# Kernel tuning notes

Hardware: AMD Instinct MI355X
Metric: run time of the kernel (lower is better)

## Reference

```python
import jax, jax.numpy as jnp
import numpy as np

D_MODEL = 1024
NHEAD = 8
HEAD_DIM = D_MODEL // NHEAD
D_FF = 4096
EPS_ATTN = 1e-6
EPS_LN = 1e-5


def _layernorm(x, g, b):
    mu = jnp.mean(x, axis=-1, keepdims=True)
    var = jnp.var(x, axis=-1, keepdims=True)
    return (x - mu) * jax.lax.rsqrt(var + EPS_LN) * g + b


def _linear_attention(q, k, v):
    # q,k,v: [N, L, H, D]
    Q = jax.nn.elu(q) + 1.0
    K = jax.nn.elu(k) + 1.0
    v_length = v.shape[1]
    v = v / v_length
    KV = jnp.einsum('nshd,nshv->nhdv', K, v)           # [N,H,D,D]
    Z = 1.0 / (jnp.einsum('nlhd,nhd->nlh', Q, K.sum(axis=1)) + EPS_ATTN)
    out = jnp.einsum('nlhd,nhdv,nlh->nlhv', Q, KV, Z) * v_length
    return out


def setup_inputs() -> dict:
    key = jax.random.key(0)
    ks = jax.random.split(key, 12)
    s = 1.0 / np.sqrt(D_MODEL)
    sf = 1.0 / np.sqrt(D_FF)
    return {
        'x': jax.random.normal(ks[0], (2, 4096, D_MODEL), jnp.float32),
        'wq': jax.random.normal(ks[1], (D_MODEL, D_MODEL), jnp.float32) * s,
        'wk': jax.random.normal(ks[2], (D_MODEL, D_MODEL), jnp.float32) * s,
        'wv': jax.random.normal(ks[3], (D_MODEL, D_MODEL), jnp.float32) * s,
        'w1': jax.random.normal(ks[4], (D_FF, D_MODEL), jnp.float32) * s,
        'b1': jnp.zeros((D_FF,), jnp.float32),
        'w2': jax.random.normal(ks[5], (D_MODEL, D_FF), jnp.float32) * sf,
        'b2': jnp.zeros((D_MODEL,), jnp.float32),
        'g1': jnp.ones((D_MODEL,), jnp.float32),
        'be1': jnp.zeros((D_MODEL,), jnp.float32),
        'g2': jnp.ones((D_MODEL,), jnp.float32),
        'be2': jnp.zeros((D_MODEL,), jnp.float32),
    }


def reference(x, wq, wk, wv, w1, b1, w2, b2, g1, be1, g2, be2):
    N, L, C = x.shape
    # pre-norm self attention
    x2 = _layernorm(x, g1, be1)
    q = (x2 @ wq.T).reshape(N, L, NHEAD, HEAD_DIM)
    k = (x2 @ wk.T).reshape(N, L, NHEAD, HEAD_DIM)
    v = (x2 @ wv.T).reshape(N, L, NHEAD, HEAD_DIM)
    msg = _linear_attention(q, k, v).reshape(N, L, C)
    x = x + msg
    # MLP block
    x2 = _layernorm(x, g2, be2)
    h = jax.nn.gelu(x2 @ w1.T + b1, approximate=False)
    x = x + (h @ w2.T + b2)
    return x
```

## Files before the change

kernel.cpp:

```cpp
#include <hip/hip_runtime.h>
#include <hip/hip_bf16.h>
#include <math.h>

typedef __bf16 bf16x8 __attribute__((ext_vector_type(8)));
typedef float f32x4 __attribute__((ext_vector_type(4)));

#define DEVI __device__ __forceinline__

DEVI void gload_lds16(const __bf16* g, __bf16* l) {
    __builtin_amdgcn_global_load_lds(
        (const __attribute__((address_space(1))) void*)g,
        (__attribute__((address_space(3))) void*)l, 16, 0, 0);
}

__global__ void sniff_kernel(const unsigned short* __restrict__ x, int* flags) {
    const int tid = threadIdx.x;
    const unsigned short u = x[tid * 2];
    const int e = (u >> 7) & 0xFF;
    const int zero = (u == 0) ? 1 : 0;
    const int sane = ((e >= 0x71 && e <= 0x8E) || ((u & 0x7FFF) == 0)) ? 1 : 0;
    const unsigned long long mz = __ballot(zero != 0);
    const unsigned long long ms = __ballot(sane != 0);
    __shared__ int wz[4], wsn[4];
    if ((tid & 63) == 0) { wz[tid >> 6] = __popcll(mz); wsn[tid >> 6] = __popcll(ms); }
    __syncthreads();
    if (tid == 0) {
        const int nz = wz[0] + wz[1] + wz[2] + wz[3];
        const int ns = wsn[0] + wsn[1] + wsn[2] + wsn[3];
        flags[0] = (nz >= 192 || ns < 128) ? 1 : 0;
    }
}

__global__ __launch_bounds__(256) void convert_kernel(const void* __restrict__ src,
                                                      __bf16* __restrict__ dst, int n,
                                                      const int* __restrict__ flags) {
    const int i = (blockIdx.x * 256 + threadIdx.x) * 8;
    if (i >= n) return;
    if (flags[0]) {
        const float* s = (const float*)src;
        bf16x8 o;
#pragma unroll
        for (int j = 0; j < 8; j++) o[j] = (__bf16)s[i + j];
        *(bf16x8*)(dst + i) = o;
    } else {
        *(uint4*)(dst + i) = *(const uint4*)((const __bf16*)src + i);
    }
}

template <typename T>
__global__ __launch_bounds__(256) void ln_kernel(const T* __restrict__ x,
                                                 const __bf16* __restrict__ g,
                                                 const __bf16* __restrict__ b,
                                                 __bf16* __restrict__ out) {
    const size_t row = blockIdx.x;
    const T* xr = x + row * 1024;
    const int tid = threadIdx.x;
    float v[4];
#pragma unroll
    for (int i = 0; i < 4; i++) v[i] = (float)xr[tid * 4 + i];
    float s = v[0] + v[1] + v[2] + v[3];
    float s2 = v[0] * v[0] + v[1] * v[1] + v[2] * v[2] + v[3] * v[3];
#pragma unroll
    for (int m = 32; m >= 1; m >>= 1) {
        s += __shfl_xor(s, m, 64);
        s2 += __shfl_xor(s2, m, 64);
    }
    __shared__ float rs[4], rs2[4];
    const int wave = tid >> 6, lane = tid & 63;
    if (lane == 0) { rs[wave] = s; rs2[wave] = s2; }
    __syncthreads();
    s = rs[0] + rs[1] + rs[2] + rs[3];
    s2 = rs2[0] + rs2[1] + rs2[2] + rs2[3];
    const float mu = s * (1.0f / 1024.0f);
    const float var = s2 * (1.0f / 1024.0f) - mu * mu;
    const float inv = rsqrtf(var + 1e-5f);
#pragma unroll
    for (int i = 0; i < 4; i++) {
        const int c = tid * 4 + i;
        out[row * 1024 + c] = (__bf16)((v[i] - mu) * inv * (float)g[c] + (float)b[c]);
    }
}

enum { EP_NONE = 0, EP_ELU1 = 1, EP_BIAS_GELU = 2, EP_BIAS_RES = 3, EP_QKV = 4 };

#define STG256(DST, P0, P1, KOFF)                         \
    do {                                                  \
        gload_lds16((P0) + (KOFF), &DST[tid * 8]);        \
        gload_lds16((P1) + (KOFF), &DST[4096 + tid * 8]); \
    } while (0)

#define MFMA4x4(AV, BV, FRB)                                                   \
    do {                                                                       \
        _Pragma("unroll") for (int f_ = 0; f_ < 4; f_++)                       \
            _Pragma("unroll") for (int c_ = 0; c_ < 4; c_++)                   \
                acc[(FRB) + f_][c_] = __builtin_amdgcn_mfma_f32_16x16x32_bf16( \
                    AV[f_], BV[c_], acc[(FRB) + f_][c_], 0, 0, 0);             \
    } while (0)

#define ITER256(RA0, RA1, RB0, RB1, SA0m, SA1m, SB0m, SB1m, TN, DO_STAGE, VM1) \
    do {                                                                       \
        bf16x8 a_[4];                                                          \
                                    \
        asm volatile("s_waitcnt vmcnt(4)" ::: "memory");                       \
        __builtin_amdgcn_s_barrier();                                          \
        __builtin_amdgcn_sched_barrier(0);                                     \
        _Pragma("unroll") for (int f_ = 0; f_ < 4; f_++)                       \
            b0[f_] = *(const bf16x8*)&RB0[boff[f_]];                           \
        _Pragma("unroll") for (int f_ = 0; f_ < 4; f_++)                       \
            a_[f_] = *(const bf16x8*)&RA0[aoff[f_]];                           \
        if (DO_STAGE) STG256(SA0m, sA0, sA1, (TN) * 64);                       \
        asm volatile("s_waitcnt lgkmcnt(0)" ::: "memory");                     \
        __builtin_amdgcn_sched_barrier(0);                                     \
        __builtin_amdgcn_s_setprio(1);                                         \
        MFMA4x4(a_, b0, 0);                                                    \
        __builtin_amdgcn_s_setprio(0);                                         \
                                    \
        asm volatile("s_waitcnt vmcnt(" #VM1 ")" ::: "memory");                \
        __builtin_amdgcn_s_barrier();                                          \
        __builtin_amdgcn_sched_barrier(0);                                     \
        _Pragma("unroll") for (int f_ = 0; f_ < 4; f_++)                       \
            b1[f_] = *(const bf16x8*)&RB1[boff[f_]];                           \
        _Pragma("unroll") for (int f_ = 0; f_ < 4; f_++)                       \
            a_[f_] = *(const bf16x8*)&RA1[aoff[f_]];                           \
        if (DO_STAGE) STG256(SB0m, sB0, sB1, (TN) * 64);                       \
        asm volatile("s_waitcnt lgkmcnt(0)" ::: "memory");                     \
        __builtin_amdgcn_sched_barrier(0);                                     \
        __builtin_amdgcn_s_setprio(1);                                         \
        MFMA4x4(a_, b1, 0);                                                    \
        __builtin_amdgcn_s_setprio(0);                                         \
                              \
        __builtin_amdgcn_s_barrier();                                          \
        __builtin_amdgcn_sched_barrier(0);                                     \
        _Pragma("unroll") for (int f_ = 0; f_ < 4; f_++)                       \
            a_[f_] = *(const bf16x8*)&RA0[aoff[4 + f_]];                       \
        if (DO_STAGE) STG256(SA1m, sA0, sA1, (TN) * 64 + 32);                  \
        asm volatile("s_waitcnt lgkmcnt(0)" ::: "memory");                     \
        __builtin_amdgcn_sched_barrier(0);                                     \
        __builtin_amdgcn_s_setprio(1);                                         \
        MFMA4x4(a_, b0, 4);                                                    \
        __builtin_amdgcn_s_setprio(0);                                         \
                              \
        __builtin_amdgcn_s_barrier();                                          \
        __builtin_amdgcn_sched_barrier(0);                                     \
        _Pragma("unroll") for (int f_ = 0; f_ < 4; f_++)                       \
            a_[f_] = *(const bf16x8*)&RA1[aoff[4 + f_]];                       \
        if (DO_STAGE) STG256(SB1m, sB0, sB1, (TN) * 64 + 32);                  \
        asm volatile("s_waitcnt lgkmcnt(0)" ::: "memory");                     \
        __builtin_amdgcn_sched_barrier(0);                                     \
        __builtin_amdgcn_s_setprio(1);                                         \
        MFMA4x4(a_, b1, 4);                                                    \
        __builtin_amdgcn_s_setprio(0);                                         \
    } while (0)

template <int EP>
__global__ __launch_bounds__(512, 2) void gemm256(
    const __bf16* __restrict__ A, const __bf16* __restrict__ B,
    const __bf16* __restrict__ bias, __bf16* __restrict__ out2,
    __bf16* __restrict__ out3, __bf16* __restrict__ C, int M, int N, int K) {
    const int gx = gridDim.x, gy = gridDim.y;
    int bm = blockIdx.y, bn = blockIdx.x;
    {
        const int nwg = gx * gy;
        const int bid = bm * gx + bn;
        if ((gx & 7) == 0 && (nwg & 63) == 0) {
            const int perx = nwg >> 3;
            const int gid = (bid & 7) * perx + (bid >> 3);
            const int stg = gid >> 6, pos = gid & 63;
            const int stw = gx >> 3;
            bm = (stg / stw) * 8 + (pos >> 3);
            bn = (stg % stw) * 8 + (pos & 7);
        } else if ((nwg & 7) == 0) {
            const int perx = nwg >> 3;
            const int gid = (bid & 7) * perx + (bid >> 3);
            bm = gid / gx;
            bn = gid % gx;
        }
    }
    const int tid = threadIdx.x;
    const int wave = tid >> 6, lane = tid & 63;
    const int wr = wave >> 2, wc = wave & 3;
    const int lm = lane & 15, lq = lane >> 4;

    __shared__ __align__(16) __bf16 A0k0[8192];
    __shared__ __align__(16) __bf16 A0k1[8192];
    __shared__ __align__(16) __bf16 B0k0[8192];
    __shared__ __align__(16) __bf16 B0k1[8192];
    __shared__ __align__(16) __bf16 A1k0[8192];
    __shared__ __align__(16) __bf16 A1k1[8192];
    __shared__ __align__(16) __bf16 B1k0[8192];
    __shared__ __align__(16) __bf16 B1k1[8192];

    f32x4 acc[8][4] = {};
    bf16x8 b0[4], b1[4];

    int aoff[8], boff[4];
#pragma unroll
    for (int fr = 0; fr < 8; fr++) {
        const int row = wr * 128 + fr * 16 + lm;
        aoff[fr] = row * 32 + ((lq ^ (lm & 3)) << 3);
    }
#pragma unroll
    for (int fc = 0; fc < 4; fc++) {
        const int row = wc * 64 + fc * 16 + lm;
        boff[fc] = row * 32 + ((lq ^ (lm & 3)) << 3);
    }

    const int srow = tid >> 2;
    const int sg = (((tid & 3) ^ ((tid >> 2) & 3)) << 3);
    const __bf16* sA0 = A + (size_t)(bm * 256 + srow) * K + sg;
    const __bf16* sA1 = sA0 + (size_t)128 * K;
    const __bf16* sB0 = B + (size_t)(bn * 256 + srow) * K + sg;
    const __bf16* sB1 = sB0 + (size_t)128 * K;

    const int nt = K >> 6;

    STG256(A0k0, sA0, sA1, 0);
    STG256(B0k0, sB0, sB1, 0);
    STG256(A0k1, sA0, sA1, 32);
    STG256(B0k1, sB0, sB1, 32);

    int t = 0;
    for (; t + 2 < nt; t += 2) {
        ITER256(A0k0, A0k1, B0k0, B0k1, A1k0, A1k1, B1k0, B1k1, t + 1, true, 2);
        ITER256(A1k0, A1k1, B1k0, B1k1, A0k0, A0k1, B0k0, B0k1, t + 2, true, 2);
    }
    ITER256(A0k0, A0k1, B0k0, B0k1, A1k0, A1k1, B1k0, B1k1, t + 1, true, 2);
    ITER256(A1k0, A1k1, B1k0, B1k1, A0k0, A0k1, B0k0, B0k1, 0, false, 0);

    const int rowb = bm * 256 + wr * 128 + lq * 4;
    const int colb = bn * 256 + wc * 64 + lm;
#pragma unroll
    for (int fr = 0; fr < 8; fr++) {
#pragma unroll
        for (int fc = 0; fc < 4; fc++) {
            const int col = colb + fc * 16;
#pragma unroll
            for (int r = 0; r < 4; r++) {
                const int row = rowb + fr * 16 + r;
                float v = acc[fr][fc][r];
                if (EP == EP_QKV) {
                    float vv = (col < 2048) ? ((v > 0.0f) ? (v + 1.0f) : expf(v)) : v;
                    __bf16* dst = (col < 1024) ? C : (col < 2048) ? out2 : out3;
                    dst[(size_t)row * 1024 + (col & 1023)] = (__bf16)vv;
                } else {
                    v += (float)bias[col];
                    v = 0.5f * v * (1.0f + erff(v * 0.70710678118654752f));
                    C[(size_t)row * N + col] = (__bf16)v;
                }
            }
        }
    }
}

#define READMM(RA, RB)                                                           \
    do {                                                                         \
        bf16x8 af_[4], bfv_[4];                                                  \
        _Pragma("unroll") for (int i_ = 0; i_ < 4; i_++) {                       \
            af_[i_] = *(const bf16x8*)&RA[(wm * 64 + i_ * 16 + lm) * 32 + swz];  \
            bfv_[i_] = *(const bf16x8*)&RB[(wn * 64 + i_ * 16 + lm) * 32 + swz]; \
        }                                                                        \
        _Pragma("unroll") for (int i_ = 0; i_ < 4; i_++)                         \
            _Pragma("unroll") for (int j_ = 0; j_ < 4; j_++)                     \
                acc[i_][j_] = __builtin_amdgcn_mfma_f32_16x16x32_bf16(           \
                    af_[i_], bfv_[j_], acc[i_][j_], 0, 0, 0);                    \
    } while (0)

#define KBODY(RA, RB, SA, SB, TS, WAITN)                           \
    do {                                                           \
        asm volatile("s_waitcnt vmcnt(" #WAITN ")" ::: "memory");  \
        __builtin_amdgcn_s_barrier();                              \
        __builtin_amdgcn_sched_barrier(0);                         \
        if ((TS) < nt) {                                           \
            const int k0_ = (TS) << 5;                             \
            gload_lds16(pa0 + k0_, &SA[tid * 8]);                  \
            gload_lds16(pa1 + k0_, &SA[2048 + tid * 8]);           \
            gload_lds16(pb0 + k0_, &SB[tid * 8]);                  \
            gload_lds16(pb1 + k0_, &SB[2048 + tid * 8]);           \
        }                                                          \
        __builtin_amdgcn_s_setprio(1);                             \
        READMM(RA, RB);                                            \
        __builtin_amdgcn_s_setprio(0);                             \
    } while (0)

template <int EP, typename OutT>
__global__ __launch_bounds__(256, 3) void gemm_bt(
    const __bf16* __restrict__ A, const __bf16* __restrict__ B,
    const __bf16* __restrict__ bias, const float* __restrict__ resid,
    OutT* __restrict__ C, int M, int N, int K) {
    const int gx = gridDim.x, gy = gridDim.y;
    int bm = blockIdx.y, bn = blockIdx.x;
    {
        const int nwg = gx * gy;
        if ((gx & 7) == 0 && (nwg & 63) == 0) {
            const int bid = bm * gx + bn;
            const int perx = nwg >> 3;
            const int gid = (bid & 7) * perx + (bid >> 3);
            const int stg = gid >> 6, pos = gid & 63;
            const int stw = gx >> 3;
            bm = (stg / stw) * 8 + (pos >> 3);
            bn = (stg % stw) * 8 + (pos & 7);
        }
    }
    const int tid = threadIdx.x;
    const int wave = tid >> 6, lane = tid & 63;
    const int wm = wave & 1, wn = wave >> 1;
    const int lm = lane & 15, lq = lane >> 4;
    const int swz = (lq ^ ((lm >> 1) & 3)) * 8;

    __shared__ __align__(16) __bf16 As0[128 * 32];
    __shared__ __align__(16) __bf16 As1[128 * 32];
    __shared__ __align__(16) __bf16 As2[128 * 32];
    __shared__ __align__(16) __bf16 Bs0[128 * 32];
    __shared__ __align__(16) __bf16 Bs1[128 * 32];
    __shared__ __align__(16) __bf16 Bs2[128 * 32];

    f32x4 acc[4][4] = {};

    const int sr = tid >> 2;
    const int sc = (((tid & 3) ^ ((tid >> 3) & 3)) << 3);

    const __bf16* pa0 = A + (size_t)(bm * 128 + sr) * K + sc;
    const __bf16* pa1 = pa0 + (size_t)64 * K;
    const __bf16* pb0 = B + (size_t)(bn * 128 + sr) * K + sc;
    const __bf16* pb1 = pb0 + (size_t)64 * K;

    const int nt = K >> 5;

    gload_lds16(pa0, &As0[tid * 8]);
    gload_lds16(pa1, &As0[2048 + tid * 8]);
    gload_lds16(pb0, &Bs0[tid * 8]);
    gload_lds16(pb1, &Bs0[2048 + tid * 8]);
    if (nt > 1) {
        gload_lds16(pa0 + 32, &As1[tid * 8]);
        gload_lds16(pa1 + 32, &As1[2048 + tid * 8]);
        gload_lds16(pb0 + 32, &Bs1[tid * 8]);
        gload_lds16(pb1 + 32, &Bs1[2048 + tid * 8]);
    }

    int t = 0;
    for (; t + 2 < nt; t += 3) {
        KBODY(As0, Bs0, As2, Bs2, t + 2, 4);
        KBODY(As1, Bs1, As0, Bs0, t + 3, 4);
        KBODY(As2, Bs2, As1, Bs1, t + 4, 4);
    }
    if (t < nt) {
        asm volatile("s_waitcnt vmcnt(0)" ::: "memory");
        __builtin_amdgcn_s_barrier();
        __builtin_amdgcn_sched_barrier(0);
        READMM(As0, Bs0);
        t++;
        if (t < nt) { READMM(As1, Bs1); }
    }

    const int row0 = bm * 128 + wm * 64;
    const int col0 = bn * 128 + wn * 64;
#pragma unroll
    for (int i = 0; i < 4; i++) {
#pragma unroll
        for (int j = 0; j < 4; j++) {
            const int col = col0 + j * 16 + lm;
#pragma unroll
            for (int r = 0; r < 4; r++) {
                const int row = row0 + i * 16 + lq * 4 + r;
                float v = acc[i][j][r];
                if (EP == EP_ELU1) {
                    v = (v > 0.0f) ? (v + 1.0f) : expf(v);
                } else if (EP == EP_BIAS_GELU) {
                    v += (float)bias[col];
                    v = 0.5f * v * (1.0f + erff(v * 0.70710678118654752f));
                } else if (EP == EP_BIAS_RES) {
                    v += (float)bias[col];
                    v += resid[(size_t)row * N + col];
                }
                C[(size_t)row * N + col] = (OutT)v;
            }
        }
    }
}

__global__ __launch_bounds__(256) void kv_kernel(const __bf16* __restrict__ Kf,
                                                 const __bf16* __restrict__ Vf,
                                                 float* __restrict__ pkv,
                                                 float* __restrict__ pks) {
    const int nh = blockIdx.x, sc = blockIdx.y;
    const int n = nh >> 3, h = nh & 7;
    const int tid = threadIdx.x;
    const int tv = tid & 15, td = tid >> 4;
    __shared__ __align__(16) __bf16 Kt[32 * 128];
    __shared__ __align__(16) __bf16 Vt[32 * 128];
    float acc[8][8] = {};
    float ks[8] = {};
    const size_t rowbase = (size_t)n * 4096 + (size_t)sc * 256;
    for (int s0 = 0; s0 < 256; s0 += 32) {
#pragma unroll
        for (int rep = 0; rep < 2; rep++) {
            const int s = tid + rep * 256;
            const int r = s >> 4, cs = (s & 15) * 8;
            const size_t gidx = (rowbase + s0 + r) * 1024 + h * 128 + cs;
            *(bf16x8*)&Kt[r * 128 + cs] = *(const bf16x8*)&Kf[gidx];
            *(bf16x8*)&Vt[r * 128 + cs] = *(const bf16x8*)&Vf[gidx];
        }
        __syncthreads();
#pragma unroll 4
        for (int s = 0; s < 32; s++) {
            const bf16x8 k8 = *(const bf16x8*)&Kt[s * 128 + td * 8];
            const bf16x8 v8 = *(const bf16x8*)&Vt[s * 128 + tv * 8];
            float kk[8], vv[8];
#pragma unroll
            for (int i = 0; i < 8; i++) { kk[i] = (float)k8[i]; vv[i] = (float)v8[i]; }
#pragma unroll
            for (int i = 0; i < 8; i++) {
                ks[i] += kk[i];
#pragma unroll
                for (int j = 0; j < 8; j++) acc[i][j] += kk[i] * vv[j];
            }
        }
        __syncthreads();
    }
    float* dst = pkv + ((size_t)sc * 16 + nh) * 16384;
#pragma unroll
    for (int i = 0; i < 8; i++)
#pragma unroll
        for (int j = 0; j < 8; j++)
            dst[(td * 8 + i) * 128 + tv * 8 + j] = acc[i][j];
    if (tv == 0) {
        float* ds2 = pks + ((size_t)sc * 16 + nh) * 128;
#pragma unroll
        for (int i = 0; i < 8; i++) ds2[td * 8 + i] = ks[i];
    }
}

__global__ __launch_bounds__(256) void kv_reduce(const float* __restrict__ pkv,
                                                 const float* __restrict__ pks,
                                                 __bf16* __restrict__ kvb,
                                                 float* __restrict__ ksf) {
    const int idx = blockIdx.x * 256 + threadIdx.x;
    float s = 0.0f;
#pragma unroll
    for (int c = 0; c < 16; c++) s += pkv[(size_t)c * 262144 + idx];
    kvb[idx] = (__bf16)s;
    if (idx < 2048) {
        float t = 0.0f;
#pragma unroll
        for (int c = 0; c < 16; c++) t += pks[c * 2048 + idx];
        ksf[idx] = t;
    }
}

__global__ __launch_bounds__(256) void z_kernel(const __bf16* __restrict__ Qf,
                                                const float* __restrict__ ksf,
                                                float* __restrict__ zbuf) {
    const int idx = blockIdx.x * 256 + threadIdx.x;
    const int h = idx & 7;
    const size_t row = (size_t)(idx >> 3);
    const __bf16* q = Qf + row * 1024 + h * 128;
    const float* ks = ksf + ((size_t)((row >> 12) * 8 + h)) * 128;
    float s = 0.0f;
    for (int d = 0; d < 128; d += 8) {
        const bf16x8 q8 = *(const bf16x8*)&q[d];
#pragma unroll
        for (int j = 0; j < 8; j++) s += (float)q8[j] * ks[d + j];
    }
    zbuf[idx] = 1.0f / (s + 1e-6f);
}

__global__ __launch_bounds__(256, 2) void attn_out_kernel(
    const __bf16* __restrict__ x, const __bf16* __restrict__ Qf,
    const __bf16* __restrict__ kvb, const float* __restrict__ zbuf,
    float* __restrict__ xmid) {
    const int nh = blockIdx.x, lc = blockIdx.y;
    const int n = nh >> 3, h = nh & 7;
    const int tid = threadIdx.x;
    __shared__ __align__(16) __bf16 KVs[128 * 128];
    __shared__ __align__(16) __bf16 Qs[64 * 128];
    __shared__ float Zs[64];
    const __bf16* kv = kvb + (size_t)nh * 16384;
    for (int i = tid * 8; i < 16384; i += 2048)
        *(bf16x8*)&KVs[i] = *(const bf16x8*)&kv[i];
    const size_t gr0 = (size_t)n * 4096 + (size_t)lc * 64;
#pragma unroll
    for (int rep = 0; rep < 4; rep++) {
        const int s = tid + rep * 256;
        const int r = s >> 4, cs = (s & 15) * 8;
        *(bf16x8*)&Qs[r * 128 + cs] = *(const bf16x8*)&Qf[(gr0 + r) * 1024 + h * 128 + cs];
    }
    if (tid < 64) Zs[tid] = zbuf[(gr0 + tid) * 8 + h];
    __syncthreads();
    const int tv = (tid & 15) * 8;
    const int tr0 = (tid >> 4) * 4;
    float acc[4][8] = {};
    for (int d = 0; d < 128; d++) {
        const bf16x8 kv8 = *(const bf16x8*)&KVs[d * 128 + tv];
        float kf[8];
#pragma unroll
        for (int j = 0; j < 8; j++) kf[j] = (float)kv8[j];
#pragma unroll
        for (int rr = 0; rr < 4; rr++) {
            const float q = (float)Qs[(tr0 + rr) * 128 + d];
#pragma unroll
            for (int j = 0; j < 8; j++) acc[rr][j] += q * kf[j];
        }
    }
#pragma unroll
    for (int rr = 0; rr < 4; rr++) {
        const size_t gi = (gr0 + tr0 + rr) * 1024 + h * 128 + tv;
        const float z = Zs[tr0 + rr];
        const bf16x8 xr = *(const bf16x8*)&x[gi];
#pragma unroll
        for (int j = 0; j < 8; j++) xmid[gi + j] = (float)xr[j] + acc[rr][j] * z;
    }
}

extern "C" void kernel_launch(void* const* d_in, const int* in_sizes, int n_in,
                              void* d_out, int out_size, void* d_ws, size_t ws_size,
                              hipStream_t stream) {
    float* out = (float*)d_out;
    char* ws = (char*)d_ws;

    const int nx = 8388608, nw = 1048576, nw1 = 4194304, nb1 = 4096, ng = 1024;
    size_t off = 0;
    __bf16* cx   = (__bf16*)(ws + off); off += (size_t)nx * 2;
    __bf16* cwq  = (__bf16*)(ws + off); off += (size_t)nw * 2;
    __bf16* cwk  = (__bf16*)(ws + off); off += (size_t)nw * 2;
    __bf16* cwv  = (__bf16*)(ws + off); off += (size_t)nw * 2;
    __bf16* cw1  = (__bf16*)(ws + off); off += (size_t)nw1 * 2;
    __bf16* cb1  = (__bf16*)(ws + off); off += (size_t)nb1 * 2;
    __bf16* cw2  = (__bf16*)(ws + off); off += (size_t)nw1 * 2;
    __bf16* cb2  = (__bf16*)(ws + off); off += (size_t)ng * 2;
    __bf16* cg1  = (__bf16*)(ws + off); off += (size_t)ng * 2;
    __bf16* cbe1 = (__bf16*)(ws + off); off += (size_t)ng * 2;
    __bf16* cg2  = (__bf16*)(ws + off); off += (size_t)ng * 2;
    __bf16* cbe2 = (__bf16*)(ws + off); off += (size_t)ng * 2;
    int* flags = (int*)(ws + off); off += 64;

    char* PB = ws + off;
    __bf16* x2   = (__bf16*)(PB);
    __bf16* Qf   = (__bf16*)(PB + 16777216);
    float*  pkv  = (float*)(PB + 33554432);
    __bf16* hbuf = (__bf16*)(PB + 16777216);
    __bf16* Kf   = (__bf16*)(PB + 50331648);
    __bf16* Vf   = (__bf16*)(PB + 67108864);
    float*  xmid = (float*)(PB + 50331648);
    float*  pks  = (float*)(PB + 83886080);
    float*  ksf  = (float*)(PB + 84017152);
    float*  zbuf = (float*)(PB + 84025344);
    __bf16* kvb  = (__bf16*)(PB + 84287488);

    sniff_kernel<<<1, 256, 0, stream>>>((const unsigned short*)d_in[0], flags);
    convert_kernel<<<nx / 2048, 256, 0, stream>>>(d_in[0], cx, nx, flags);
    convert_kernel<<<nw / 2048, 256, 0, stream>>>(d_in[1], cwq, nw, flags);
    convert_kernel<<<nw / 2048, 256, 0, stream>>>(d_in[2], cwk, nw, flags);
    convert_kernel<<<nw / 2048, 256, 0, stream>>>(d_in[3], cwv, nw, flags);
    convert_kernel<<<nw1 / 2048, 256, 0, stream>>>(d_in[4], cw1, nw1, flags);
    convert_kernel<<<2, 256, 0, stream>>>(d_in[5], cb1, nb1, flags);
    convert_kernel<<<nw1 / 2048, 256, 0, stream>>>(d_in[6], cw2, nw1, flags);
    convert_kernel<<<1, 256, 0, stream>>>(d_in[7], cb2, ng, flags);
    convert_kernel<<<1, 256, 0, stream>>>(d_in[8], cg1, ng, flags);
    convert_kernel<<<1, 256, 0, stream>>>(d_in[9], cbe1, ng, flags);
    convert_kernel<<<1, 256, 0, stream>>>(d_in[10], cg2, ng, flags);
    convert_kernel<<<1, 256, 0, stream>>>(d_in[11], cbe2, ng, flags);

    ln_kernel<__bf16><<<8192, 256, 0, stream>>>(cx, cg1, cbe1, x2);
    gemm256<EP_QKV><<<dim3(3072 / 256, 8192 / 256), 512, 0, stream>>>(
        x2, cwq, nullptr, Kf, Vf, Qf, 8192, 3072, 1024);
    kv_kernel<<<dim3(16, 16), 256, 0, stream>>>(Kf, Vf, pkv, pks);
    kv_reduce<<<1024, 256, 0, stream>>>(pkv, pks, kvb, ksf);
    z_kernel<<<256, 256, 0, stream>>>(Qf, ksf, zbuf);
    attn_out_kernel<<<dim3(16, 64), 256, 0, stream>>>(cx, Qf, kvb, zbuf, xmid);
    ln_kernel<float><<<8192, 256, 0, stream>>>(xmid, cg2, cbe2, x2);
    for (int c = 0; c < 2; c++) {
        const size_t ro = (size_t)c * 4096;
        gemm256<EP_BIAS_GELU><<<dim3(4096 / 256, 4096 / 256), 512, 0, stream>>>(
            x2 + ro * 1024, cw1, cb1, nullptr, nullptr, hbuf, 4096, 4096, 1024);
        gemm_bt<EP_BIAS_RES, float><<<dim3(1024 / 128, 4096 / 128), 256, 0, stream>>>(
            hbuf, cw2, cb2, xmid + ro * 1024, out + ro * 1024, 4096, 1024, 4096);
    }
}
```

Baseline: 465.0 us.

## Restructure GEMM pipeline barriers and change LDS swizzle pattern

Reorders the per-iteration schedule of the 256x256 bf16 GEMM so LDS fragment reads and global-to-LDS staging are issued before the vmcnt wait and workgroup barrier, and adds a barrier after each MFMA phase. It also changes the staging order of the A/B k-halves and moves the first vmcnt wait out of the loop. Separately, the XOR swizzle on LDS rows now uses (row>>1)&3 instead of row&3, aiming to cut LDS bank conflicts for 16-byte reads. The extra barriers add synchronisation cost, and the reordered waits could break correctness if the vmcnt counts do not match the outstanding loads.

New measurement: 463.4 us. Within noise of the previous version (-0.4%).

```diff
diff --git a/kernel.cpp b/kernel.cpp
--- a/kernel.cpp
+++ b/kernel.cpp
@@ -97,59 +97,68 @@
                     AV[f_], BV[c_], acc[(FRB) + f_][c_], 0, 0, 0);             \
     } while (0)
 
-#define ITER256(RA0, RA1, RB0, RB1, SA0m, SA1m, SB0m, SB1m, TN, DO_STAGE, VM1) \
+#define BAR()                                  \
+    do {                                       \
+        __builtin_amdgcn_sched_barrier(0);     \
+        __builtin_amdgcn_s_barrier();          \
+        __builtin_amdgcn_sched_barrier(0);     \
+    } while (0)
+
+#define LGKM0()                                                \
+    do {                                                       \
+        asm volatile("s_waitcnt lgkmcnt(0)" ::: "memory");     \
+        __builtin_amdgcn_sched_barrier(0);                     \
+    } while (0)
+
+#define ITER256(RA0, RA1, RB0, RB1, SA0m, SB0m, SA1m, SB1m, TN, DO_STAGE, VM0, VM3) \
     do {                                                                       \
         bf16x8 a_[4];                                                          \
-                                    \
-        asm volatile("s_waitcnt vmcnt(4)" ::: "memory");                       \
-        __builtin_amdgcn_s_barrier();                                          \
-        __builtin_amdgcn_sched_barrier(0);                                     \
+                          \
         _Pragma("unroll") for (int f_ = 0; f_ < 4; f_++)                       \
             b0[f_] = *(const bf16x8*)&RB0[boff[f_]];                           \
         _Pragma("unroll") for (int f_ = 0; f_ < 4; f_++)                       \
             a_[f_] = *(const bf16x8*)&RA0[aoff[f_]];                           \
         if (DO_STAGE) STG256(SA0m, sA0, sA1, (TN) * 64);                       \
-        asm volatile("s_waitcnt lgkmcnt(0)" ::: "memory");                     \
-        __builtin_amdgcn_sched_barrier(0);                                     \
+        asm volatile("s_waitcnt vmcnt(" #VM0 ")" ::: "memory");                \
+        BAR();                                                                 \
+        LGKM0();                                                               \
         __builtin_amdgcn_s_setprio(1);                                         \
         MFMA4x4(a_, b0, 0);                                                    \
         __builtin_amdgcn_s_setprio(0);                                         \
-                                    \
-        asm volatile("s_waitcnt vmcnt(" #VM1 ")" ::: "memory");                \
-        __builtin_amdgcn_s_barrier();                                          \
-        __builtin_amdgcn_sched_barrier(0);                                     \
+        BAR();                                                                 \
+                          \
         _Pragma("unroll") for (int f_ = 0; f_ < 4; f_++)                       \
             b1[f_] = *(const bf16x8*)&RB1[boff[f_]];                           \
         _Pragma("unroll") for (int f_ = 0; f_ < 4; f_++)                       \
             a_[f_] = *(const bf16x8*)&RA1[aoff[f_]];                           \
         if (DO_STAGE) STG256(SB0m, sB0, sB1, (TN) * 64);                       \
-        asm volatile("s_waitcnt lgkmcnt(0)" ::: "memory");                     \
-        __builtin_amdgcn_sched_barrier(0);                                     \
+        BAR();                                                                 \
+        LGKM0();                                                               \
         __builtin_amdgcn_s_setprio(1);                                         \
         MFMA4x4(a_, b1, 0);                                                    \
         __builtin_amdgcn_s_setprio(0);                                         \
-                              \
-        __builtin_amdgcn_s_barrier();                                          \
-        __builtin_amdgcn_sched_barrier(0);                                     \
+        BAR();                                                                 \
+                         \
         _Pragma("unroll") for (int f_ = 0; f_ < 4; f_++)                       \
             a_[f_] = *(const bf16x8*)&RA0[aoff[4 + f_]];                       \
         if (DO_STAGE) STG256(SA1m, sA0, sA1, (TN) * 64 + 32);                  \
-        asm volatile("s_waitcnt lgkmcnt(0)" ::: "memory");                     \
-        __builtin_amdgcn_sched_barrier(0);                                     \
+        BAR();                                                                 \
+        LGKM0();                                                               \
         __builtin_amdgcn_s_setprio(1);                                         \
         MFMA4x4(a_, b0, 4);                                                    \
         __builtin_amdgcn_s_setprio(0);                                         \
-                              \
-        __builtin_amdgcn_s_barrier();                                          \
-        __builtin_amdgcn_sched_barrier(0);                                     \
+        BAR();                                                                 \
+                         \
         _Pragma("unroll") for (int f_ = 0; f_ < 4; f_++)                       \
             a_[f_] = *(const bf16x8*)&RA1[aoff[4 + f_]];                       \
         if (DO_STAGE) STG256(SB1m, sB0, sB1, (TN) * 64 + 32);                  \
-        asm volatile("s_waitcnt lgkmcnt(0)" ::: "memory");                     \
-        __builtin_amdgcn_sched_barrier(0);                                     \
+        asm volatile("s_waitcnt vmcnt(" #VM3 ")" ::: "memory");                \
+        BAR();                                                                 \
+        LGKM0();                                                               \
         __builtin_amdgcn_s_setprio(1);                                         \
         MFMA4x4(a_, b1, 4);                                                    \
         __builtin_amdgcn_s_setprio(0);                                         \
+        BAR();                                                                 \
     } while (0)
 
 template <int EP>
@@ -197,16 +206,16 @@
 #pragma unroll
     for (int fr = 0; fr < 8; fr++) {
         const int row = wr * 128 + fr * 16 + lm;
-        aoff[fr] = row * 32 + ((lq ^ (lm & 3)) << 3);
+        aoff[fr] = row * 32 + ((lq ^ ((lm >> 1) & 3)) << 3);
     }
 #pragma unroll
     for (int fc = 0; fc < 4; fc++) {
         const int row = wc * 64 + fc * 16 + lm;
-        boff[fc] = row * 32 + ((lq ^ (lm & 3)) << 3);
+        boff[fc] = row * 32 + ((lq ^ ((lm >> 1) & 3)) << 3);
     }
 
     const int srow = tid >> 2;
-    const int sg = (((tid & 3) ^ ((tid >> 2) & 3)) << 3);
+    const int sg = (((tid & 3) ^ ((tid >> 3) & 3)) << 3);
     const __bf16* sA0 = A + (size_t)(bm * 256 + srow) * K + sg;
     const __bf16* sA1 = sA0 + (size_t)128 * K;
     const __bf16* sB0 = B + (size_t)(bn * 256 + srow) * K + sg;
@@ -218,14 +227,16 @@
     STG256(B0k0, sB0, sB1, 0);
     STG256(A0k1, sA0, sA1, 32);
     STG256(B0k1, sB0, sB1, 32);
+    asm volatile("s_waitcnt vmcnt(4)" ::: "memory");
+    BAR();
 
     int t = 0;
     for (; t + 2 < nt; t += 2) {
-        ITER256(A0k0, A0k1, B0k0, B0k1, A1k0, A1k1, B1k0, B1k1, t + 1, true, 2);
-        ITER256(A1k0, A1k1, B1k0, B1k1, A0k0, A0k1, B0k0, B0k1, t + 2, true, 2);
-    }
-    ITER256(A0k0, A0k1, B0k0, B0k1, A1k0, A1k1, B1k0, B1k1, t + 1, true, 2);
-    ITER256(A1k0, A1k1, B1k0, B1k1, A0k0, A0k1, B0k0, B0k1, 0, false, 0);
+        ITER256(A0k0, A0k1, B0k0, B0k1, A1k0, B1k0, A1k1, B1k1, t + 1, true, 2, 4);
+        ITER256(A1k0, A1k1, B1k0, B1k1, A0k0, B0k0, A0k1, B0k1, t + 2, true, 2, 4);
+    }
+    ITER256(A0k0, A0k1, B0k0, B0k1, A1k0, B1k0, A1k1, B1k1, t + 1, true, 2, 4);
+    ITER256(A1k0, A1k1, B1k0, B1k1, A0k0, B0k0, A0k1, B0k1, 0, false, 0, 0);
 
     const int rowb = bm * 256 + wr * 128 + lq * 4;
     const int colb = bn * 256 + wc * 64 + lm;
```
